# Performance work log

Hardware: AMD Instinct MI355X
Metric: run time of the kernel (lower is better)

The kernel has to match this reference:

```python
import jax, jax.numpy as jnp
import numpy as np

B, SQ, SK = 2, 2048, 2048
QDIM = KDIM = HID = 1024
H = 16
DH = HID // H  # inner_dim = 64


def setup_inputs() -> dict:
    key = jax.random.key(0)
    ks = jax.random.split(key, 8)
    q = jax.random.normal(ks[0], (B, SQ, QDIM), dtype=jnp.float32)
    k = jax.random.normal(ks[1], (B, SK, KDIM), dtype=jnp.float32)
    v = jax.random.normal(ks[2], (B, SK, KDIM), dtype=jnp.float32)
    mask = jax.random.randint(ks[3], (B, SQ, SK), 0, 2).astype(jnp.bool_)
    scale = 1.0 / np.sqrt(QDIM)
    # per-head projections, stored stacked: [H, in_dim, DH]
    Wq = jax.random.normal(ks[4], (H, QDIM, DH), dtype=jnp.float32) * scale
    Wk = jax.random.normal(ks[5], (H, KDIM, DH), dtype=jnp.float32) * scale
    Wv = jax.random.normal(ks[6], (H, KDIM, DH), dtype=jnp.float32) * scale
    Wo = jax.random.normal(ks[7], (HID, QDIM), dtype=jnp.float32) * scale
    return {"q": q, "k": k, "v": v, "mask": mask,
            "Wq": Wq, "Wk": Wk, "Wv": Wv, "Wo": Wo}


def reference(q, k, v, mask, Wq, Wk, Wv, Wo):
    dh = Wq.shape[-1]
    qh = jnp.einsum('bsd,hde->bhse', q, Wq)   # [B,H,SQ,DH]
    kh = jnp.einsum('bsd,hde->bhse', k, Wk)   # [B,H,SK,DH]
    vh = jnp.einsum('bsd,hde->bhse', v, Wv)   # [B,H,SK,DH]
    scores = jnp.einsum('bhqd,bhkd->bhqk', qh, kh) / jnp.sqrt(jnp.asarray(dh, qh.dtype))
    scores = jnp.where(mask[:, None, :, :], -jnp.inf, scores)
    attn = jax.nn.softmax(scores, axis=-1)
    att = jnp.einsum('bhqk,bhkd->bhqd', attn, vh)        # [B,H,SQ,DH]
    concat = att.transpose(0, 2, 1, 3).reshape(q.shape[0], q.shape[1], -1)  # head-order concat
    return concat @ Wo  # [B,SQ,QDIM]
```

## Files before the change

### kernel.cpp

```cpp
#include <hip/hip_runtime.h>

#define NB 2
#define NH 16
#define SEQ 2048
#define DMODEL 1024
#define DHEAD 64
#define QSCALE 0.18033688f

typedef __attribute__((ext_vector_type(8))) short bf16x8;
typedef __attribute__((ext_vector_type(4))) short bf16x4;
typedef __attribute__((ext_vector_type(4))) float f32x4;
typedef __attribute__((ext_vector_type(16))) float f32x16;
typedef __attribute__((ext_vector_type(4))) int i32x4;

static __device__ __forceinline__ unsigned short f2bf(float f) {
    unsigned int u = __float_as_uint(f);
    u += 0x7fffu + ((u >> 16) & 1u);
    return (unsigned short)(u >> 16);
}
static __device__ __forceinline__ unsigned int pk2(float lo, float hi) {
    return (unsigned int)f2bf(lo) | ((unsigned int)f2bf(hi) << 16);
}
static __device__ __forceinline__ void gld_lds16(const unsigned short* g, unsigned short* l) {
    __builtin_amdgcn_global_load_lds(
        (const __attribute__((address_space(1))) unsigned int*)g,
        (__attribute__((address_space(3))) unsigned int*)l, 16, 0, 0);
}

__global__ __launch_bounds__(256) void prep_kernel(
    const int* __restrict__ mask, unsigned long long* __restrict__ mpack,
    const float* __restrict__ Wq, const float* __restrict__ Wk, const float* __restrict__ Wv,
    unsigned short* __restrict__ Wqt, unsigned short* __restrict__ Wkt,
    unsigned short* __restrict__ Wvt,
    const float* __restrict__ Wo, unsigned short* __restrict__ Wot,
    const float* __restrict__ q, const float* __restrict__ k, const float* __restrict__ v,
    unsigned short* __restrict__ qb, unsigned short* __restrict__ kb,
    unsigned short* __restrict__ vb)
{
    __shared__ __align__(16) float Ls[64][65];
    const int bid = blockIdx.x, t = threadIdx.x;

    if (bid < 1024) {
        const int wave = bid * 4 + (t >> 6);
        const int lane = t & 63;
        const int* row = mask + (size_t)wave * SEQ;
        unsigned long long* orow = mpack + (size_t)wave * (SEQ / 64);
        for (int w = 0; w < SEQ / 64; ++w) {
            int m = row[w * 64 + lane];
            unsigned long long bits = __ballot(m != 0);
            if (lane == 0) orow[w] = bits;
        }
    } else if (bid < 2048) {
        const float* S; unsigned short* D; float scale; int R, tile_r, tile_c, ostride;
        if (bid < 1792) {
            const int local = bid - 1024, z = local >> 4, sel = z >> 4, h = z & 15;
            S = (sel == 0 ? Wq : sel == 1 ? Wk : Wv) + (size_t)h * DMODEL * DHEAD;
            D = (sel == 0 ? Wqt : sel == 1 ? Wkt : Wvt) + (size_t)h * DMODEL * DHEAD;
            scale = (sel == 0) ? QSCALE : 1.0f;
            tile_r = (local & 15) * 64; tile_c = 0; R = DHEAD; ostride = DMODEL;
        } else {
            const int local = bid - 1792;
            S = Wo; D = Wot; scale = 1.0f;
            tile_c = (local & 15) * 64; tile_r = (local >> 4) * 64; R = DMODEL; ostride = DMODEL;
        }
        const int c4 = (t & 15) * 4;
        for (int rr = t >> 4; rr < 64; rr += 16) {
            float4 x = *(const float4*)(S + (size_t)(tile_r + rr) * R + tile_c + c4);
            Ls[rr][c4 + 0] = x.x; Ls[rr][c4 + 1] = x.y;
            Ls[rr][c4 + 2] = x.z; Ls[rr][c4 + 3] = x.w;
        }
        __syncthreads();
        const int r4 = (t & 15) * 4;
        for (int cc = t >> 4; cc < 64; cc += 16) {
            ushort4 o;
            o.x = f2bf(Ls[r4 + 0][cc] * scale); o.y = f2bf(Ls[r4 + 1][cc] * scale);
            o.z = f2bf(Ls[r4 + 2][cc] * scale); o.w = f2bf(Ls[r4 + 3][cc] * scale);
            *(ushort4*)(D + (size_t)(tile_c + cc) * ostride + tile_r + r4) = o;
        }
    } else {
        const int local = bid - 2048;
        const int z = local >> 11;
        const float* S = (z == 0) ? q : (z == 1) ? k : v;
        unsigned short* D = (z == 0) ? qb : (z == 1) ? kb : vb;
        const size_t i = ((size_t)(local & 2047) * 256 + t) * 8;
        float4 x0 = *(const float4*)(S + i);
        float4 x1 = *(const float4*)(S + i + 4);
        uint4 val;
        val.x = pk2(x0.x, x0.y); val.y = pk2(x0.z, x0.w);
        val.z = pk2(x1.x, x1.y); val.w = pk2(x1.z, x1.w);
        *(uint4*)(D + i) = val;
    }
}

__global__ __launch_bounds__(256) void proj_gemm_kernel(
    const unsigned short* __restrict__ qb, const unsigned short* __restrict__ kb,
    const unsigned short* __restrict__ vb,
    const unsigned short* __restrict__ Wqt, const unsigned short* __restrict__ Wkt,
    const unsigned short* __restrict__ Wvt,
    unsigned short* __restrict__ qh, unsigned short* __restrict__ kh,
    unsigned short* __restrict__ vt)
{
    const int bid = blockIdx.x;
    const int sx = bid >> 3;
    const int mtg = (bid & 7) * 12 + (sx >> 3);
    const int z = mtg >> 5;
    const int m0 = (mtg & 31) * 128;
    const int n0 = (sx & 7) * 128;

    const unsigned short* A = (z == 0) ? qb : (z == 1) ? kb : vb;
    const unsigned short* Bt = (z == 0) ? Wqt : (z == 1) ? Wkt : Wvt;

    const int t = threadIdx.x, lane = t & 63, w = t >> 6;
    const int lg = lane >> 4, ln = lane & 15;
    const int wx = w & 1, wy = w >> 1;

    __shared__ __align__(16) unsigned short SM[17408];
    unsigned short* As = SM;
    unsigned short* Bs = SM + 8192;

    f32x4 acc[4][4] = {};

    for (int kk = 0; kk < DMODEL; kk += 64) {
        #pragma unroll
        for (int i = 0; i < 4; ++i) {
            int s = (w * 4 + i) * 64 + lane;
            int n = s >> 3, c = (s & 7) ^ (n & 7);
            gld_lds16(Bt + (size_t)(n0 + n) * DMODEL + kk + c * 8, Bs + (size_t)s * 8);
        }
        #pragma unroll
        for (int i = 0; i < 4; ++i) {
            int s = (w * 4 + i) * 64 + lane;
            int n = s >> 3, c = (s & 7) ^ (n & 7);
            gld_lds16(A + (size_t)(m0 + n) * DMODEL + kk + c * 8, As + (size_t)s * 8);
        }
        __syncthreads();
        #pragma unroll
        for (int ks = 0; ks < 2; ++ks) {
            bf16x8 af[4], bf[4];
            #pragma unroll
            for (int rb = 0; rb < 4; ++rb) {
                int r = wy * 64 + rb * 16 + ln;
                af[rb] = *(const bf16x8*)(As + r * 64 + (((ks * 4 + lg) ^ (r & 7)) * 8));
            }
            #pragma unroll
            for (int nb = 0; nb < 4; ++nb) {
                int n = wx * 64 + nb * 16 + ln;
                bf[nb] = *(const bf16x8*)(Bs + n * 64 + (((ks * 4 + lg) ^ (n & 7)) * 8));
            }
            #pragma unroll
            for (int rb = 0; rb < 4; ++rb)
                #pragma unroll
                for (int nb = 0; nb < 4; ++nb)
                    acc[rb][nb] = __builtin_amdgcn_mfma_f32_16x16x32_bf16(
                        af[rb], bf[nb], acc[rb][nb], 0, 0, 0);
        }
        __syncthreads();
    }

    if (z < 2) {
        unsigned short* Y = (z == 0) ? qh : kh;
        unsigned short* Ep = SM;
        #pragma unroll
        for (int rb = 0; rb < 4; ++rb)
            #pragma unroll
            for (int nb = 0; nb < 4; ++nb) {
                const int c_l = wx * 64 + nb * 16 + ln;
                const int base = ((c_l >> 6) << 13) + (c_l & 63);
                #pragma unroll
                for (int r = 0; r < 4; ++r) {
                    const int s_l = wy * 64 + rb * 16 + lg * 4 + r;
                    Ep[base + s_l * 64] = f2bf(acc[rb][nb][r]);
                }
            }
        __syncthreads();
        {
            const int head = t >> 7, r2 = t & 127;
            const unsigned short* src = Ep + head * 8192 + r2 * 64;
            unsigned short* dst = Y + ((size_t)((m0 >> 11) * NH + (n0 >> 6) + head) * SEQ
                                       + (m0 & (SEQ - 1)) + r2) * DHEAD;
            #pragma unroll
            for (int i = 0; i < 8; ++i)
                *(uint4*)(dst + i * 8) = *(const uint4*)(src + i * 8);
        }
    } else {
        unsigned short* Ep = SM;
        #pragma unroll
        for (int rb = 0; rb < 4; ++rb)
            #pragma unroll
            for (int nb = 0; nb < 4; ++nb) {
                const int c_l = wx * 64 + nb * 16 + ln;
                const int seq0 = wy * 64 + rb * 16 + lg * 4;
                ushort4 o;
                o.x = f2bf(acc[rb][nb][0]); o.y = f2bf(acc[rb][nb][1]);
                o.z = f2bf(acc[rb][nb][2]); o.w = f2bf(acc[rb][nb][3]);
                *(ushort4*)(Ep + (c_l >> 6) * 8704 + (c_l & 63) * 136 + seq0) = o;
            }
        __syncthreads();
        {
            const int head = t >> 7, dh = (t >> 1) & 63, hf = t & 1;
            const unsigned short* src = Ep + head * 8704 + dh * 136 + hf * 64;
            unsigned short* dst = vt
                + ((size_t)((((m0 >> 11) << 4) + (n0 >> 6) + head) * DHEAD + dh) * SEQ
                   + (m0 & (SEQ - 1)) + hf * 64);
            #pragma unroll
            for (int i = 0; i < 8; ++i)
                *(uint4*)(dst + i * 8) = *(const uint4*)(src + i * 8);
        }
    }
}

__global__ __launch_bounds__(512, 4) void attn_kernel(
    const unsigned short* __restrict__ qh, const unsigned short* __restrict__ kh,
    const unsigned short* __restrict__ vt, const unsigned long long* __restrict__ mpack,
    unsigned short* __restrict__ att)
{
    const int t = threadIdx.x, lane = t & 63;
    const int w8 = t >> 6;
    const int half = w8 >> 2, w = w8 & 3;
    const int th = t & 255;
    const int h = lane >> 5, lq = lane & 31;
    const int L = lq & 7, X = (lq >> 3) & 3;

    const int bid = blockIdx.x;
    const int r_ = bid >> 3;
    const int qt = r_ & 15;
    const int bh = (bid & 7) * 4 + (r_ >> 4);
    const int b = bh >> 4, hd = bh & 15;
    const int row0 = qt * 128;
    const int qrow = row0 + w * 32 + lq;
    const int kt0 = half * (SEQ / 2);

    __shared__ __align__(16) unsigned short SMEM[2 * 16384];
    unsigned short* Kh = SMEM + half * 16384;
    unsigned short* Vh = Kh + 8192;

    const unsigned short* Kb = kh + (size_t)bh * SEQ * DHEAD;
    const unsigned short* Vb = vt + (size_t)bh * DHEAD * SEQ;

    const unsigned short* Qb = qh + ((size_t)bh * SEQ + qrow) * DHEAD;
    bf16x8 qf[4];
    #pragma unroll
    for (int d = 0; d < 4; ++d) qf[d] = *(const bf16x8*)(Qb + d * 16 + h * 8);

    const unsigned long long* Mb = mpack + ((size_t)b * SEQ + qrow) * (SEQ / 64);

    int oK[2], oV[2], sL[2];
    #pragma unroll
    for (int i = 0; i < 2; ++i) {
        const int s = i * 256 + th;
        const int n = s >> 3, c = (s & 7) ^ (n & 7) ^ ((n >> 3) & 3);
        sL[i] = s * 8;
        oK[i] = n * DHEAD + c * 8;
        oV[i] = n * SEQ + c * 8;
    }

    f32x16 acc[2] = {};
    f32x16 lacc = {};
    bf16x8 ones;
    #pragma unroll
    for (int i = 0; i < 8; ++i) ones[i] = (short)0x3f80;

    unsigned long long mw, mwn = 0;

    #pragma unroll
    for (int i = 0; i < 2; ++i)
        gld_lds16(Kb + (size_t)kt0 * DHEAD + oK[i], Kh + sL[i]);
    #pragma unroll
    for (int i = 0; i < 2; ++i)
        gld_lds16(Vb + (size_t)kt0 + oV[i], Vh + sL[i]);
    mw = Mb[half << 4];
    __syncthreads();

    for (int tix = 0; tix < 16; ++tix) {
        const int buf = tix & 1;

        if (tix < 15) {
            const int ktn = kt0 + (tix + 1) * 64;
            unsigned short* Kd = Kh + (buf ^ 1) * 4096;
            unsigned short* Vd = Vh + (buf ^ 1) * 4096;
            #pragma unroll
            for (int i = 0; i < 2; ++i)
                gld_lds16(Kb + (size_t)ktn * DHEAD + oK[i], Kd + sL[i]);
            #pragma unroll
            for (int i = 0; i < 2; ++i)
                gld_lds16(Vb + (size_t)ktn + oV[i], Vd + sL[i]);
            mwn = Mb[(half << 4) + tix + 1];
        }

        const unsigned short* Ksb = Kh + buf * 4096;
        const unsigned short* Vsb = Vh + buf * 4096;
        const unsigned long long mh_ = mw >> (h * 4);

        #pragma unroll
        for (int st = 0; st < 2; ++st) {
            f32x16 S = {};
            __builtin_amdgcn_s_setprio(1);
            #pragma unroll
            for (int d = 0; d < 4; ++d) {
                bf16x8 kf = *(const bf16x8*)(Ksb + (st * 32 + lq) * 64
                                             + (((d * 2 + h) ^ L ^ X) * 8));
                S = __builtin_amdgcn_mfma_f32_32x32x16_bf16(kf, qf[d], S, 0, 0, 0);
            }
            __builtin_amdgcn_s_setprio(0);
            const unsigned int wn = ~(unsigned int)(mh_ >> (32 * st));
            unsigned int pd[8];
            #pragma unroll
            for (int bb = 0; bb < 4; ++bb) {
                float e[4];
                #pragma unroll
                for (int rr = 0; rr < 4; ++rr) {
                    const int keep = __builtin_amdgcn_sbfe(wn, 8 * bb + rr, 1);
                    float ex = __builtin_amdgcn_exp2f(S[bb * 4 + rr]);
                    e[rr] = __uint_as_float(__float_as_uint(ex) & (unsigned int)keep);
                }
                pd[bb * 2 + 0] = __builtin_amdgcn_perm(
                    __float_as_uint(e[1]), __float_as_uint(e[0]), 0x07060302u);
                pd[bb * 2 + 1] = __builtin_amdgcn_perm(
                    __float_as_uint(e[3]), __float_as_uint(e[2]), 0x07060302u);
            }
            #pragma unroll
            for (int k2 = 0; k2 < 2; ++k2) {
                i32x4 pi = { (int)pd[4 * k2 + 0], (int)pd[4 * k2 + 1],
                             (int)pd[4 * k2 + 2], (int)pd[4 * k2 + 3] };
                bf16x8 pf = __builtin_bit_cast(bf16x8, pi);
                const int p0 = (((4 * st + 2 * k2) ^ L ^ X)) * 8;
                bf16x8 vf0, vf1;
                {
                    const unsigned short* vb_ = Vsb + lq * 64 + 4 * h;
                    bf16x4 a0 = *(const bf16x4*)(vb_ + p0);
                    bf16x4 a1 = *(const bf16x4*)(vb_ + (p0 ^ 8));
                    vf0 = __builtin_shufflevector(a0, a1, 0, 1, 2, 3, 4, 5, 6, 7);
                    const unsigned short* vc_ = vb_ + 32 * 64;
                    bf16x4 c0 = *(const bf16x4*)(vc_ + p0);
                    bf16x4 c1 = *(const bf16x4*)(vc_ + (p0 ^ 8));
                    vf1 = __builtin_shufflevector(c0, c1, 0, 1, 2, 3, 4, 5, 6, 7);
                }
                __builtin_amdgcn_s_setprio(1);
                lacc = __builtin_amdgcn_mfma_f32_32x32x16_bf16(ones, pf, lacc, 0, 0, 0);
                acc[0] = __builtin_amdgcn_mfma_f32_32x32x16_bf16(vf0, pf, acc[0], 0, 0, 0);
                acc[1] = __builtin_amdgcn_mfma_f32_32x32x16_bf16(vf1, pf, acc[1], 0, 0, 0);
                __builtin_amdgcn_s_setprio(0);
            }
        }

        mw = mwn;
        __syncthreads();
    }

    const int rloc = w * 32 + lq;
    float* Osh = (float*)SMEM;
    float* Lsh = (float*)SMEM + 128 * 68;

    if (half == 1) {
        #pragma unroll
        for (int dt = 0; dt < 2; ++dt)
            #pragma unroll
            for (int g = 0; g < 4; ++g) {
                f32x4 v = { acc[dt][g * 4 + 0], acc[dt][g * 4 + 1],
                            acc[dt][g * 4 + 2], acc[dt][g * 4 + 3] };
                *(f32x4*)(Osh + rloc * 68 + dt * 32 + 8 * g + 4 * h) = v;
            }
        if (h == 0) Lsh[rloc] = lacc[0];
    }
    __syncthreads();
    if (half == 0) {
        const float linv = 1.0f / (lacc[0] + Lsh[rloc]);
        unsigned short* Ar = att + ((size_t)b * SEQ + qrow) * DMODEL + hd * DHEAD;
        #pragma unroll
        for (int dt = 0; dt < 2; ++dt)
            #pragma unroll
            for (int g = 0; g < 4; ++g) {
                const int dh0 = dt * 32 + 8 * g + 4 * h;
                f32x4 p = *(const f32x4*)(Osh + rloc * 68 + dh0);
                ushort4 o;
                o.x = f2bf((acc[dt][g * 4 + 0] + p[0]) * linv);
                o.y = f2bf((acc[dt][g * 4 + 1] + p[1]) * linv);
                o.z = f2bf((acc[dt][g * 4 + 2] + p[2]) * linv);
                o.w = f2bf((acc[dt][g * 4 + 3] + p[3]) * linv);
                *(ushort4*)(Ar + dh0) = o;
            }
    }
}

__global__ __launch_bounds__(256) void out_gemm_kernel(
    const unsigned short* __restrict__ A, const unsigned short* __restrict__ Bt,
    float* __restrict__ C)
{
    const int bid = blockIdx.x;
    const int sx = bid >> 3;
    const int m0 = ((bid & 7) * 8 + (sx >> 3)) * 64;
    const int n0 = (sx & 7) * 128;

    const int t = threadIdx.x, lane = t & 63, w = t >> 6;
    const int lg = lane >> 4, ln = lane & 15;
    const int wx = w & 1, wy = w >> 1;

    __shared__ __align__(16) unsigned short As[64 * 64];
    __shared__ __align__(16) unsigned short Bs[128 * 64];

    f32x4 acc[2][4] = {};

    for (int kk = 0; kk < DMODEL; kk += 64) {
        #pragma unroll
        for (int i = 0; i < 4; ++i) {
            int s = (w * 4 + i) * 64 + lane;
            int n = s >> 3, c = (s & 7) ^ (n & 7);
            gld_lds16(Bt + (size_t)(n0 + n) * DMODEL + kk + c * 8, Bs + (size_t)s * 8);
        }
        #pragma unroll
        for (int i = 0; i < 2; ++i) {
            int s = (w * 2 + i) * 64 + lane;
            int n = s >> 3, c = (s & 7) ^ (n & 7);
            gld_lds16(A + (size_t)(m0 + n) * DMODEL + kk + c * 8, As + (size_t)s * 8);
        }
        __syncthreads();
        #pragma unroll
        for (int ks = 0; ks < 2; ++ks) {
            bf16x8 af[2], bf[4];
            #pragma unroll
            for (int rb = 0; rb < 2; ++rb) {
                int r = wy * 32 + rb * 16 + ln;
                af[rb] = *(const bf16x8*)(As + r * 64 + (((ks * 4 + lg) ^ (r & 7)) * 8));
            }
            #pragma unroll
            for (int nb = 0; nb < 4; ++nb) {
                int n = wx * 64 + nb * 16 + ln;
                bf[nb] = *(const bf16x8*)(Bs + n * 64 + (((ks * 4 + lg) ^ (n & 7)) * 8));
            }
            #pragma unroll
            for (int rb = 0; rb < 2; ++rb)
                #pragma unroll
                for (int nb = 0; nb < 4; ++nb)
                    acc[rb][nb] = __builtin_amdgcn_mfma_f32_16x16x32_bf16(
                        af[rb], bf[nb], acc[rb][nb], 0, 0, 0);
        }
        __syncthreads();
    }

    #pragma unroll
    for (int rb = 0; rb < 2; ++rb)
        #pragma unroll
        for (int nb = 0; nb < 4; ++nb)
            #pragma unroll
            for (int r = 0; r < 4; ++r) {
                int grow = m0 + wy * 32 + rb * 16 + lg * 4 + r;
                int gcol = n0 + wx * 64 + nb * 16 + ln;
                C[(size_t)grow * DMODEL + gcol] = acc[rb][nb][r];
            }
}

extern "C" void kernel_launch(void* const* d_in, const int* in_sizes, int n_in,
                              void* d_out, int out_size, void* d_ws, size_t ws_size,
                              hipStream_t stream) {
    const float* q    = (const float*)d_in[0];
    const float* k    = (const float*)d_in[1];
    const float* v    = (const float*)d_in[2];
    const int*   mask = (const int*)  d_in[3];
    const float* Wq   = (const float*)d_in[4];
    const float* Wk   = (const float*)d_in[5];
    const float* Wv   = (const float*)d_in[6];
    const float* Wo   = (const float*)d_in[7];
    float* out = (float*)d_out;

    unsigned short* ws  = (unsigned short*)d_ws;
    const size_t n1 = (size_t)NB * NH * SEQ * DHEAD;
    const size_t nw = (size_t)NH * DHEAD * DMODEL;
    unsigned short* qh  = ws;
    unsigned short* kh  = qh + n1;
    unsigned short* vt  = kh + n1;
    unsigned short* att = vt + n1;
    unsigned short* Wqt = att + n1;
    unsigned short* Wkt = Wqt + nw;
    unsigned short* Wvt = Wkt + nw;
    unsigned short* Wot = Wvt + nw;
    unsigned long long* mpack = (unsigned long long*)(Wot + nw);
    unsigned short* regA = (unsigned short*)(mpack + (size_t)NB * SEQ * (SEQ / 64));
    unsigned short* qb = regA;
    unsigned short* kb = qb + n1;
    unsigned short* vb = kb + n1;

    prep_kernel<<<dim3(8192), 256, 0, stream>>>(
        mask, mpack, Wq, Wk, Wv, Wqt, Wkt, Wvt, Wo, Wot, q, k, v, qb, kb, vb);
    proj_gemm_kernel<<<dim3(768), 256, 0, stream>>>(qb, kb, vb, Wqt, Wkt, Wvt, qh, kh, vt);
    attn_kernel<<<dim3(512), 512, 0, stream>>>(qh, kh, vt, mpack, att);
    out_gemm_kernel<<<dim3(512), 256, 0, stream>>>(att, Wot, out);
}
```

Before: 256.6 us.

## Double-buffer LDS tiles in projection and output GEMMs, shrink projection tiles

```diff
diff --git a/kernel.cpp b/kernel.cpp
--- a/kernel.cpp
+++ b/kernel.cpp
@@ -100,111 +100,117 @@
     unsigned short* __restrict__ qh, unsigned short* __restrict__ kh,
     unsigned short* __restrict__ vt)
 {
-    const int bid = blockIdx.x;
-    const int sx = bid >> 3;
-    const int mtg = (bid & 7) * 12 + (sx >> 3);
-    const int z = mtg >> 5;
-    const int m0 = (mtg & 31) * 128;
-    const int n0 = (sx & 7) * 128;
-
-    const unsigned short* A = (z == 0) ? qb : (z == 1) ? kb : vb;
-    const unsigned short* Bt = (z == 0) ? Wqt : (z == 1) ? Wkt : Wvt;
-
     const int t = threadIdx.x, lane = t & 63, w = t >> 6;
     const int lg = lane >> 4, ln = lane & 15;
     const int wx = w & 1, wy = w >> 1;
 
-    __shared__ __align__(16) unsigned short SM[17408];
-    unsigned short* As = SM;
-    unsigned short* Bs = SM + 8192;
-
-    f32x4 acc[4][4] = {};
-
-    for (int kk = 0; kk < DMODEL; kk += 64) {
-        #pragma unroll
-        for (int i = 0; i < 4; ++i) {
-            int s = (w * 4 + i) * 64 + lane;
-            int n = s >> 3, c = (s & 7) ^ (n & 7);
-            gld_lds16(Bt + (size_t)(n0 + n) * DMODEL + kk + c * 8, Bs + (size_t)s * 8);
-        }
-        #pragma unroll
-        for (int i = 0; i < 4; ++i) {
-            int s = (w * 4 + i) * 64 + lane;
-            int n = s >> 3, c = (s & 7) ^ (n & 7);
-            gld_lds16(A + (size_t)(m0 + n) * DMODEL + kk + c * 8, As + (size_t)s * 8);
+    __shared__ __align__(16) unsigned short SM[24576];
+
+    #pragma unroll 1
+    for (int vi = 0; vi < 2; ++vi) {
+        const int vti = blockIdx.x + vi * 768;
+        const int z = vti >> 9;
+        const int r = vti & 511;
+        const int m0 = ((r & 7) * 8 + (r >> 6)) * 64;
+        const int n0 = ((r >> 3) & 7) * 128;
+
+        const unsigned short* A  = (z == 0) ? qb : (z == 1) ? kb : vb;
+        const unsigned short* Bt = (z == 0) ? Wqt : (z == 1) ? Wkt : Wvt;
+
+        f32x4 acc[2][4] = {};
+
+        {
+            unsigned short* Ad = SM;
+            unsigned short* Bd = SM + 8192;
+            #pragma unroll
+            for (int i = 0; i < 4; ++i) {
+                int s = (w * 4 + i) * 64 + lane;
+                int n = s >> 3, c = (s & 7) ^ (n & 7);
+                gld_lds16(Bt + (size_t)(n0 + n) * DMODEL + c * 8, Bd + (size_t)s * 8);
+            }
+            #pragma unroll
+            for (int i = 0; i < 2; ++i) {
+                int s = (w * 2 + i) * 64 + lane;
+                int n = s >> 3, c = (s & 7) ^ (n & 7);
+                gld_lds16(A + (size_t)(m0 + n) * DMODEL + c * 8, Ad + (size_t)s * 8);
+            }
         }
         __syncthreads();
-        #pragma unroll
-        for (int ks = 0; ks < 2; ++ks) {
-            bf16x8 af[4], bf[4];
-            #pragma unroll
-            for (int rb = 0; rb < 4; ++rb) {
-                int r = wy * 64 + rb * 16 + ln;
-                af[rb] = *(const bf16x8*)(As + r * 64 + (((ks * 4 + lg) ^ (r & 7)) * 8));
-            }
-            #pragma unroll
-            for (int nb = 0; nb < 4; ++nb) {
-                int n = wx * 64 + nb * 16 + ln;
-                bf[nb] = *(const bf16x8*)(Bs + n * 64 + (((ks * 4 + lg) ^ (n & 7)) * 8));
-            }
-            #pragma unroll
-            for (int rb = 0; rb < 4; ++rb)
+
+        for (int ki = 0; ki < 16; ++ki) {
+            const int buf = ki & 1;
+
+            if (ki < 15) {
+                const int kk = (ki + 1) * 64;
+                unsigned short* Ad = SM + (buf ^ 1) * 4096;
+                unsigned short* Bd = SM + 8192 + (buf ^ 1) * 8192;
+                #pragma unroll
+                for (int i = 0; i < 4; ++i) {
+                    int s = (w * 4 + i) * 64 + lane;
+                    int n = s >> 3, c = (s & 7) ^ (n & 7);
+                    gld_lds16(Bt + (size_t)(n0 + n) * DMODEL + kk + c * 8, Bd + (size_t)s * 8);
+                }
+                #pragma unroll
+                for (int i = 0; i < 2; ++i) {
+                    int s = (w * 2 + i) * 64 + lane;
+                    int n = s >> 3, c = (s & 7) ^ (n & 7);
+                    gld_lds16(A + (size_t)(m0 + n) * DMODEL + kk + c * 8, Ad + (size_t)s * 8);
+                }
+            }
+
+            const unsigned short* Asb = SM + buf * 4096;
+            const unsigned short* Bsb = SM + 8192 + buf * 8192;
+            #pragma unroll
+            for (int ks = 0; ks < 2; ++ks) {
+                bf16x8 af[2], bf[4];
+                #pragma unroll
+                for (int rb = 0; rb < 2; ++rb) {
+                    int rr = wy * 32 + rb * 16 + ln;
+                    af[rb] = *(const bf16x8*)(Asb + rr * 64 + (((ks * 4 + lg) ^ (rr & 7)) * 8));
+                }
+                #pragma unroll
+                for (int nb = 0; nb < 4; ++nb) {
+                    int n = wx * 64 + nb * 16 + ln;
+                    bf[nb] = *(const bf16x8*)(Bsb + n * 64 + (((ks * 4 + lg) ^ (n & 7)) * 8));
+                }
+                #pragma unroll
+                for (int rb = 0; rb < 2; ++rb)
+                    #pragma unroll
+                    for (int nb = 0; nb < 4; ++nb)
+                        acc[rb][nb] = __builtin_amdgcn_mfma_f32_16x16x32_bf16(
+                            af[rb], bf[nb], acc[rb][nb], 0, 0, 0);
+            }
+            __syncthreads();
+        }
+
+        if (z < 2) {
+            unsigned short* Y = (z == 0) ? qh : kh;
+            #pragma unroll
+            for (int rb = 0; rb < 2; ++rb)
                 #pragma unroll
                 for (int nb = 0; nb < 4; ++nb)
-                    acc[rb][nb] = __builtin_amdgcn_mfma_f32_16x16x32_bf16(
-                        af[rb], bf[nb], acc[rb][nb], 0, 0, 0);
-        }
-        __syncthreads();
-    }
-
-    if (z < 2) {
-        unsigned short* Y = (z == 0) ? qh : kh;
-        unsigned short* Ep = SM;
-        #pragma unroll
-        for (int rb = 0; rb < 4; ++rb)
-            #pragma unroll
-            for (int nb = 0; nb < 4; ++nb) {
-                const int c_l = wx * 64 + nb * 16 + ln;
-                const int base = ((c_l >> 6) << 13) + (c_l & 63);
-                #pragma unroll
-                for (int r = 0; r < 4; ++r) {
-                    const int s_l = wy * 64 + rb * 16 + lg * 4 + r;
-                    Ep[base + s_l * 64] = f2bf(acc[rb][nb][r]);
-                }
-            }
-        __syncthreads();
-        {
-            const int head = t >> 7, r2 = t & 127;
-            const unsigned short* src = Ep + head * 8192 + r2 * 64;
-            unsigned short* dst = Y + ((size_t)((m0 >> 11) * NH + (n0 >> 6) + head) * SEQ
-                                       + (m0 & (SEQ - 1)) + r2) * DHEAD;
-            #pragma unroll
-            for (int i = 0; i < 8; ++i)
-                *(uint4*)(dst + i * 8) = *(const uint4*)(src + i * 8);
-        }
-    } else {
-        unsigned short* Ep = SM;
-        #pragma unroll
-        for (int rb = 0; rb < 4; ++rb)
-            #pragma unroll
-            for (int nb = 0; nb < 4; ++nb) {
-                const int c_l = wx * 64 + nb * 16 + ln;
-                const int seq0 = wy * 64 + rb * 16 + lg * 4;
-                ushort4 o;
-                o.x = f2bf(acc[rb][nb][0]); o.y = f2bf(acc[rb][nb][1]);
-                o.z = f2bf(acc[rb][nb][2]); o.w = f2bf(acc[rb][nb][3]);
-                *(ushort4*)(Ep + (c_l >> 6) * 8704 + (c_l & 63) * 136 + seq0) = o;
-            }
-        __syncthreads();
-        {
-            const int head = t >> 7, dh = (t >> 1) & 63, hf = t & 1;
-            const unsigned short* src = Ep + head * 8704 + dh * 136 + hf * 64;
-            unsigned short* dst = vt
-                + ((size_t)((((m0 >> 11) << 4) + (n0 >> 6) + head) * DHEAD + dh) * SEQ
-                   + (m0 & (SEQ - 1)) + hf * 64);
-            #pragma unroll
-            for (int i = 0; i < 8; ++i)
-                *(uint4*)(dst + i * 8) = *(const uint4*)(src + i * 8);
+                    #pragma unroll
+                    for (int rr = 0; rr < 4; ++rr) {
+                        int grow = m0 + wy * 32 + rb * 16 + lg * 4 + rr;
+                        int gcol = n0 + wx * 64 + nb * 16 + ln;
+                        size_t idx = ((size_t)((grow >> 11) * NH + (gcol >> 6)) * SEQ
+                                      + (grow & (SEQ - 1))) * DHEAD + (gcol & 63);
+                        Y[idx] = f2bf(acc[rb][nb][rr]);
+                    }
+        } else {
+            #pragma unroll
+            for (int rb = 0; rb < 2; ++rb)
+                #pragma unroll
+                for (int nb = 0; nb < 4; ++nb) {
+                    int grow0 = m0 + wy * 32 + rb * 16 + lg * 4;
+                    int gcol  = n0 + wx * 64 + nb * 16 + ln;
+                    int bh = ((grow0 >> 11) << 4) + (gcol >> 6);
+                    ushort4 st;
+                    st.x = f2bf(acc[rb][nb][0]); st.y = f2bf(acc[rb][nb][1]);
+                    st.z = f2bf(acc[rb][nb][2]); st.w = f2bf(acc[rb][nb][3]);
+                    *(ushort4*)(vt + ((size_t)bh * DHEAD + (gcol & 63)) * SEQ
+                                     + (grow0 & (SEQ - 1))) = st;
+                }
         }
     }
 }
@@ -395,37 +401,63 @@
     const int lg = lane >> 4, ln = lane & 15;
     const int wx = w & 1, wy = w >> 1;
 
-    __shared__ __align__(16) unsigned short As[64 * 64];
-    __shared__ __align__(16) unsigned short Bs[128 * 64];
+    __shared__ __align__(16) unsigned short SM[24576];
 
     f32x4 acc[2][4] = {};
 
-    for (int kk = 0; kk < DMODEL; kk += 64) {
+    {
+        unsigned short* Ad = SM;
+        unsigned short* Bd = SM + 8192;
         #pragma unroll
         for (int i = 0; i < 4; ++i) {
             int s = (w * 4 + i) * 64 + lane;
             int n = s >> 3, c = (s & 7) ^ (n & 7);
-            gld_lds16(Bt + (size_t)(n0 + n) * DMODEL + kk + c * 8, Bs + (size_t)s * 8);
+            gld_lds16(Bt + (size_t)(n0 + n) * DMODEL + c * 8, Bd + (size_t)s * 8);
         }
         #pragma unroll
         for (int i = 0; i < 2; ++i) {
             int s = (w * 2 + i) * 64 + lane;
             int n = s >> 3, c = (s & 7) ^ (n & 7);
-            gld_lds16(A + (size_t)(m0 + n) * DMODEL + kk + c * 8, As + (size_t)s * 8);
-        }
-        __syncthreads();
+            gld_lds16(A + (size_t)(m0 + n) * DMODEL + c * 8, Ad + (size_t)s * 8);
+        }
+    }
+    __syncthreads();
+
+    for (int ki = 0; ki < 16; ++ki) {
+        const int buf = ki & 1;
+
+        if (ki < 15) {
+            const int kk = (ki + 1) * 64;
+            unsigned short* Ad = SM + (buf ^ 1) * 4096;
+            unsigned short* Bd = SM + 8192 + (buf ^ 1) * 8192;
+            #pragma unroll
+            for (int i = 0; i < 4; ++i) {
+                int s = (w * 4 + i) * 64 + lane;
+                int n = s >> 3, c = (s & 7) ^ (n & 7);
+                gld_lds16(Bt + (size_t)(n0 + n) * DMODEL + kk + c * 8, Bd + (size_t)s * 8);
+            }
+            #pragma unroll
+            for (int i = 0; i < 2; ++i) {
+                int s = (w * 2 + i) * 64 + lane;
+                int n = s >> 3, c = (s & 7) ^ (n & 7);
+                gld_lds16(A + (size_t)(m0 + n) * DMODEL + kk + c * 8, Ad + (size_t)s * 8);
+            }
+        }
+
+        const unsigned short* Asb = SM + buf * 4096;
+        const unsigned short* Bsb = SM + 8192 + buf * 8192;
         #pragma unroll
         for (int ks = 0; ks < 2; ++ks) {
             bf16x8 af[2], bf[4];
             #pragma unroll
             for (int rb = 0; rb < 2; ++rb) {
-                int r = wy * 32 + rb * 16 + ln;
-                af[rb] = *(const bf16x8*)(As + r * 64 + (((ks * 4 + lg) ^ (r & 7)) * 8));
+                int rr = wy * 32 + rb * 16 + ln;
+                af[rb] = *(const bf16x8*)(Asb + rr * 64 + (((ks * 4 + lg) ^ (rr & 7)) * 8));
             }
             #pragma unroll
             for (int nb = 0; nb < 4; ++nb) {
                 int n = wx * 64 + nb * 16 + ln;
-                bf[nb] = *(const bf16x8*)(Bs + n * 64 + (((ks * 4 + lg) ^ (n & 7)) * 8));
+                bf[nb] = *(const bf16x8*)(Bsb + n * 64 + (((ks * 4 + lg) ^ (n & 7)) * 8));
             }
             #pragma unroll
             for (int rb = 0; rb < 2; ++rb)
@@ -442,10 +474,10 @@
         #pragma unroll
         for (int nb = 0; nb < 4; ++nb)
             #pragma unroll
-            for (int r = 0; r < 4; ++r) {
-                int grow = m0 + wy * 32 + rb * 16 + lg * 4 + r;
+            for (int rr = 0; rr < 4; ++rr) {
+                int grow = m0 + wy * 32 + rb * 16 + lg * 4 + rr;
                 int gcol = n0 + wx * 64 + nb * 16 + ln;
-                C[(size_t)grow * DMODEL + gcol] = acc[rb][nb][r];
+                C[(size_t)grow * DMODEL + gcol] = acc[rb][nb][rr];
             }
 }
 
@@ -474,8 +506,7 @@
     unsigned short* Wvt = Wkt + nw;
     unsigned short* Wot = Wvt + nw;
     unsigned long long* mpack = (unsigned long long*)(Wot + nw);
-    unsigned short* regA = (unsigned short*)(mpack + (size_t)NB * SEQ * (SEQ / 64));
-    unsigned short* qb = regA;
+    unsigned short* qb = (unsigned short*)(mpack + (size_t)NB * SEQ * (SEQ / 64));
     unsigned short* kb = qb + n1;
     unsigned short* vb = kb + n1;
 
```

Result: faster. 243.9 us (-4.9%).

## Fuse fp32-to-bf16 activation conversion into projection GEMM and double-buffer GEMM loads

Applied to the files above, without the earlier changes.

```diff
diff --git a/kernel.cpp b/kernel.cpp
--- a/kernel.cpp
+++ b/kernel.cpp
@@ -32,10 +32,7 @@
     const float* __restrict__ Wq, const float* __restrict__ Wk, const float* __restrict__ Wv,
     unsigned short* __restrict__ Wqt, unsigned short* __restrict__ Wkt,
     unsigned short* __restrict__ Wvt,
-    const float* __restrict__ Wo, unsigned short* __restrict__ Wot,
-    const float* __restrict__ q, const float* __restrict__ k, const float* __restrict__ v,
-    unsigned short* __restrict__ qb, unsigned short* __restrict__ kb,
-    unsigned short* __restrict__ vb)
+    const float* __restrict__ Wo, unsigned short* __restrict__ Wot)
 {
     __shared__ __align__(16) float Ls[64][65];
     const int bid = blockIdx.x, t = threadIdx.x;
@@ -50,7 +47,7 @@
             unsigned long long bits = __ballot(m != 0);
             if (lane == 0) orow[w] = bits;
         }
-    } else if (bid < 2048) {
+    } else {
         const float* S; unsigned short* D; float scale; int R, tile_r, tile_c, ostride;
         if (bid < 1792) {
             const int local = bid - 1024, z = local >> 4, sel = z >> 4, h = z & 15;
@@ -77,24 +74,12 @@
             o.z = f2bf(Ls[r4 + 2][cc] * scale); o.w = f2bf(Ls[r4 + 3][cc] * scale);
             *(ushort4*)(D + (size_t)(tile_c + cc) * ostride + tile_r + r4) = o;
         }
-    } else {
-        const int local = bid - 2048;
-        const int z = local >> 11;
-        const float* S = (z == 0) ? q : (z == 1) ? k : v;
-        unsigned short* D = (z == 0) ? qb : (z == 1) ? kb : vb;
-        const size_t i = ((size_t)(local & 2047) * 256 + t) * 8;
-        float4 x0 = *(const float4*)(S + i);
-        float4 x1 = *(const float4*)(S + i + 4);
-        uint4 val;
-        val.x = pk2(x0.x, x0.y); val.y = pk2(x0.z, x0.w);
-        val.z = pk2(x1.x, x1.y); val.w = pk2(x1.z, x1.w);
-        *(uint4*)(D + i) = val;
     }
 }
 
 __global__ __launch_bounds__(256) void proj_gemm_kernel(
-    const unsigned short* __restrict__ qb, const unsigned short* __restrict__ kb,
-    const unsigned short* __restrict__ vb,
+    const float* __restrict__ qf32, const float* __restrict__ kf32,
+    const float* __restrict__ vf32,
     const unsigned short* __restrict__ Wqt, const unsigned short* __restrict__ Wkt,
     const unsigned short* __restrict__ Wvt,
     unsigned short* __restrict__ qh, unsigned short* __restrict__ kh,
@@ -107,45 +92,81 @@
     const int m0 = (mtg & 31) * 128;
     const int n0 = (sx & 7) * 128;
 
-    const unsigned short* A = (z == 0) ? qb : (z == 1) ? kb : vb;
+    const float* Af = (z == 0) ? qf32 : (z == 1) ? kf32 : vf32;
     const unsigned short* Bt = (z == 0) ? Wqt : (z == 1) ? Wkt : Wvt;
 
     const int t = threadIdx.x, lane = t & 63, w = t >> 6;
     const int lg = lane >> 4, ln = lane & 15;
     const int wx = w & 1, wy = w >> 1;
 
-    __shared__ __align__(16) unsigned short SM[17408];
-    unsigned short* As = SM;
-    unsigned short* Bs = SM + 8192;
+    __shared__ __align__(16) unsigned short SM[32768];
+
+    int an[4], ac[4];
+    #pragma unroll
+    for (int i = 0; i < 4; ++i) {
+        const int s = i * 256 + t;
+        an[i] = s >> 3;
+        ac[i] = (s & 7) ^ (an[i] & 7);
+    }
 
     f32x4 acc[4][4] = {};
-
-    for (int kk = 0; kk < DMODEL; kk += 64) {
-        #pragma unroll
-        for (int i = 0; i < 4; ++i) {
-            int s = (w * 4 + i) * 64 + lane;
-            int n = s >> 3, c = (s & 7) ^ (n & 7);
-            gld_lds16(Bt + (size_t)(n0 + n) * DMODEL + kk + c * 8, Bs + (size_t)s * 8);
-        }
-        #pragma unroll
-        for (int i = 0; i < 4; ++i) {
-            int s = (w * 4 + i) * 64 + lane;
-            int n = s >> 3, c = (s & 7) ^ (n & 7);
-            gld_lds16(A + (size_t)(m0 + n) * DMODEL + kk + c * 8, As + (size_t)s * 8);
-        }
-        __syncthreads();
+    float4 ast[4][2];
+
+    #pragma unroll
+    for (int i = 0; i < 4; ++i) {
+        const float* src = Af + (size_t)(m0 + an[i]) * DMODEL + ac[i] * 8;
+        ast[i][0] = *(const float4*)(src);
+        ast[i][1] = *(const float4*)(src + 4);
+    }
+    #pragma unroll
+    for (int i = 0; i < 4; ++i) {
+        int s = (w * 4 + i) * 64 + lane;
+        int n = s >> 3, c = (s & 7) ^ (n & 7);
+        gld_lds16(Bt + (size_t)(n0 + n) * DMODEL + c * 8, SM + 16384 + (size_t)s * 8);
+    }
+    #pragma unroll
+    for (int i = 0; i < 4; ++i) {
+        uint4 val;
+        val.x = pk2(ast[i][0].x, ast[i][0].y); val.y = pk2(ast[i][0].z, ast[i][0].w);
+        val.z = pk2(ast[i][1].x, ast[i][1].y); val.w = pk2(ast[i][1].z, ast[i][1].w);
+        *(uint4*)(SM + (size_t)(i * 256 + t) * 8) = val;
+    }
+    __syncthreads();
+
+    for (int ki = 0; ki < 16; ++ki) {
+        const int buf = ki & 1;
+
+        if (ki < 15) {
+            const int kk = (ki + 1) * 64;
+            #pragma unroll
+            for (int i = 0; i < 4; ++i) {
+                const float* src = Af + (size_t)(m0 + an[i]) * DMODEL + kk + ac[i] * 8;
+                ast[i][0] = *(const float4*)(src);
+                ast[i][1] = *(const float4*)(src + 4);
+            }
+            #pragma unroll
+            for (int i = 0; i < 4; ++i) {
+                int s = (w * 4 + i) * 64 + lane;
+                int n = s >> 3, c = (s & 7) ^ (n & 7);
+                gld_lds16(Bt + (size_t)(n0 + n) * DMODEL + kk + c * 8,
+                          SM + 16384 + (buf ^ 1) * 8192 + (size_t)s * 8);
+            }
+        }
+
+        const unsigned short* Asb = SM + buf * 8192;
+        const unsigned short* Bsb = SM + 16384 + buf * 8192;
         #pragma unroll
         for (int ks = 0; ks < 2; ++ks) {
             bf16x8 af[4], bf[4];
             #pragma unroll
             for (int rb = 0; rb < 4; ++rb) {
                 int r = wy * 64 + rb * 16 + ln;
-                af[rb] = *(const bf16x8*)(As + r * 64 + (((ks * 4 + lg) ^ (r & 7)) * 8));
+                af[rb] = *(const bf16x8*)(Asb + r * 64 + (((ks * 4 + lg) ^ (r & 7)) * 8));
             }
             #pragma unroll
             for (int nb = 0; nb < 4; ++nb) {
                 int n = wx * 64 + nb * 16 + ln;
-                bf[nb] = *(const bf16x8*)(Bs + n * 64 + (((ks * 4 + lg) ^ (n & 7)) * 8));
+                bf[nb] = *(const bf16x8*)(Bsb + n * 64 + (((ks * 4 + lg) ^ (n & 7)) * 8));
             }
             #pragma unroll
             for (int rb = 0; rb < 4; ++rb)
@@ -153,6 +174,17 @@
                 for (int nb = 0; nb < 4; ++nb)
                     acc[rb][nb] = __builtin_amdgcn_mfma_f32_16x16x32_bf16(
                         af[rb], bf[nb], acc[rb][nb], 0, 0, 0);
+        }
+
+        if (ki < 15) {
+            unsigned short* Ad = SM + (buf ^ 1) * 8192;
+            #pragma unroll
+            for (int i = 0; i < 4; ++i) {
+                uint4 val;
+                val.x = pk2(ast[i][0].x, ast[i][0].y); val.y = pk2(ast[i][0].z, ast[i][0].w);
+                val.z = pk2(ast[i][1].x, ast[i][1].y); val.w = pk2(ast[i][1].z, ast[i][1].w);
+                *(uint4*)(Ad + (size_t)(i * 256 + t) * 8) = val;
+            }
         }
         __syncthreads();
     }
@@ -395,37 +427,63 @@
     const int lg = lane >> 4, ln = lane & 15;
     const int wx = w & 1, wy = w >> 1;
 
-    __shared__ __align__(16) unsigned short As[64 * 64];
-    __shared__ __align__(16) unsigned short Bs[128 * 64];
+    __shared__ __align__(16) unsigned short SM[24576];
 
     f32x4 acc[2][4] = {};
 
-    for (int kk = 0; kk < DMODEL; kk += 64) {
+    {
+        unsigned short* Ad = SM;
+        unsigned short* Bd = SM + 8192;
         #pragma unroll
         for (int i = 0; i < 4; ++i) {
             int s = (w * 4 + i) * 64 + lane;
             int n = s >> 3, c = (s & 7) ^ (n & 7);
-            gld_lds16(Bt + (size_t)(n0 + n) * DMODEL + kk + c * 8, Bs + (size_t)s * 8);
+            gld_lds16(Bt + (size_t)(n0 + n) * DMODEL + c * 8, Bd + (size_t)s * 8);
         }
         #pragma unroll
         for (int i = 0; i < 2; ++i) {
             int s = (w * 2 + i) * 64 + lane;
             int n = s >> 3, c = (s & 7) ^ (n & 7);
-            gld_lds16(A + (size_t)(m0 + n) * DMODEL + kk + c * 8, As + (size_t)s * 8);
-        }
-        __syncthreads();
+            gld_lds16(A + (size_t)(m0 + n) * DMODEL + c * 8, Ad + (size_t)s * 8);
+        }
+    }
+    __syncthreads();
+
+    for (int ki = 0; ki < 16; ++ki) {
+        const int buf = ki & 1;
+
+        if (ki < 15) {
+            const int kk = (ki + 1) * 64;
+            unsigned short* Ad = SM + (buf ^ 1) * 4096;
+            unsigned short* Bd = SM + 8192 + (buf ^ 1) * 8192;
+            #pragma unroll
+            for (int i = 0; i < 4; ++i) {
+                int s = (w * 4 + i) * 64 + lane;
+                int n = s >> 3, c = (s & 7) ^ (n & 7);
+                gld_lds16(Bt + (size_t)(n0 + n) * DMODEL + kk + c * 8, Bd + (size_t)s * 8);
+            }
+            #pragma unroll
+            for (int i = 0; i < 2; ++i) {
+                int s = (w * 2 + i) * 64 + lane;
+                int n = s >> 3, c = (s & 7) ^ (n & 7);
+                gld_lds16(A + (size_t)(m0 + n) * DMODEL + kk + c * 8, Ad + (size_t)s * 8);
+            }
+        }
+
+        const unsigned short* Asb = SM + buf * 4096;
+        const unsigned short* Bsb = SM + 8192 + buf * 8192;
         #pragma unroll
         for (int ks = 0; ks < 2; ++ks) {
             bf16x8 af[2], bf[4];
             #pragma unroll
             for (int rb = 0; rb < 2; ++rb) {
-                int r = wy * 32 + rb * 16 + ln;
-                af[rb] = *(const bf16x8*)(As + r * 64 + (((ks * 4 + lg) ^ (r & 7)) * 8));
+                int rr = wy * 32 + rb * 16 + ln;
+                af[rb] = *(const bf16x8*)(Asb + rr * 64 + (((ks * 4 + lg) ^ (rr & 7)) * 8));
             }
             #pragma unroll
             for (int nb = 0; nb < 4; ++nb) {
                 int n = wx * 64 + nb * 16 + ln;
-                bf[nb] = *(const bf16x8*)(Bs + n * 64 + (((ks * 4 + lg) ^ (n & 7)) * 8));
+                bf[nb] = *(const bf16x8*)(Bsb + n * 64 + (((ks * 4 + lg) ^ (n & 7)) * 8));
             }
             #pragma unroll
             for (int rb = 0; rb < 2; ++rb)
@@ -442,10 +500,10 @@
         #pragma unroll
         for (int nb = 0; nb < 4; ++nb)
             #pragma unroll
-            for (int r = 0; r < 4; ++r) {
-                int grow = m0 + wy * 32 + rb * 16 + lg * 4 + r;
+            for (int rr = 0; rr < 4; ++rr) {
+                int grow = m0 + wy * 32 + rb * 16 + lg * 4 + rr;
                 int gcol = n0 + wx * 64 + nb * 16 + ln;
-                C[(size_t)grow * DMODEL + gcol] = acc[rb][nb][r];
+                C[(size_t)grow * DMODEL + gcol] = acc[rb][nb][rr];
             }
 }
 
@@ -474,14 +532,10 @@
     unsigned short* Wvt = Wkt + nw;
     unsigned short* Wot = Wvt + nw;
     unsigned long long* mpack = (unsigned long long*)(Wot + nw);
-    unsigned short* regA = (unsigned short*)(mpack + (size_t)NB * SEQ * (SEQ / 64));
-    unsigned short* qb = regA;
-    unsigned short* kb = qb + n1;
-    unsigned short* vb = kb + n1;
-
-    prep_kernel<<<dim3(8192), 256, 0, stream>>>(
-        mask, mpack, Wq, Wk, Wv, Wqt, Wkt, Wvt, Wo, Wot, q, k, v, qb, kb, vb);
-    proj_gemm_kernel<<<dim3(768), 256, 0, stream>>>(qb, kb, vb, Wqt, Wkt, Wvt, qh, kh, vt);
+
+    prep_kernel<<<dim3(2048), 256, 0, stream>>>(
+        mask, mpack, Wq, Wk, Wv, Wqt, Wkt, Wvt, Wo, Wot);
+    proj_gemm_kernel<<<dim3(768), 256, 0, stream>>>(q, k, v, Wqt, Wkt, Wvt, qh, kh, vt);
     attn_kernel<<<dim3(512), 512, 0, stream>>>(qh, kh, vt, mpack, att);
     out_gemm_kernel<<<dim3(512), 256, 0, stream>>>(att, Wot, out);
 }
```

New measurement: 278.3 us. 1.08x slower.
